# Kernel tuning notes

Hardware: AMD Instinct MI355X
Metric: run time of the kernel (lower is better)

The kernel has to match this reference:

```python
import jax, jax.numpy as jnp
import numpy as np

N, E = 10000, 640000
IN_FT, OUT_FT = 512, 128
NEG_SLOPE = 0.2


def setup_inputs() -> dict:
    key = jax.random.key(0)
    ks = jax.random.split(key, 10)
    seq = jax.random.normal(ks[0], (N, IN_FT), dtype=jnp.float32)
    # edges with no self-loops: dst = (src + offset) % N, offset in [1, N-1]
    src = jax.random.randint(ks[1], (E,), 0, N)
    off = jax.random.randint(ks[2], (E,), 1, N)
    dst = (src + off) % N
    edge_index = jnp.stack([src, dst]).astype(jnp.int64)
    # parameters (xavier-ish scale)
    W_fc = jax.random.normal(ks[3], (OUT_FT, IN_FT), dtype=jnp.float32) * (1.0 / np.sqrt(IN_FT))
    W_gat = jax.random.normal(ks[4], (OUT_FT, OUT_FT), dtype=jnp.float32) * (1.0 / np.sqrt(OUT_FT))
    att_src = jax.random.normal(ks[5], (OUT_FT,), dtype=jnp.float32) * 0.1
    att_dst = jax.random.normal(ks[6], (OUT_FT,), dtype=jnp.float32) * 0.1
    gat_bias = jnp.zeros((OUT_FT,), dtype=jnp.float32)
    bias = jnp.zeros((OUT_FT,), dtype=jnp.float32)
    prelu_a = jnp.asarray(0.25, dtype=jnp.float32)
    return {"seq": seq, "edge_index": edge_index, "W_fc": W_fc, "W_gat": W_gat,
            "att_src": att_src, "att_dst": att_dst, "gat_bias": gat_bias,
            "bias": bias, "prelu_a": prelu_a}


def _gat_forward(seq, src, dst, W_fc, W_gat, att_src, att_dst, gat_bias, bias, prelu_a):
    n = seq.shape[0]
    x = seq @ W_fc.T                      # [N, out_ft] fc (no bias)
    h = x @ W_gat.T                       # GATConv internal linear (no bias)
    a_s = h @ att_src                     # [N] per-node src attention logits
    a_d = h @ att_dst                     # [N]
    e = a_s[src] + a_d[dst]               # [E'] per-edge raw score
    e = jnp.where(e >= 0, e, NEG_SLOPE * e)
    # segment softmax over destination node
    m = jax.ops.segment_max(e, dst, num_segments=n)
    m = jnp.where(jnp.isfinite(m), m, 0.0)
    p = jnp.exp(e - m[dst])
    denom = jax.ops.segment_sum(p, dst, num_segments=n)
    alpha = p / (denom[dst] + 1e-16)
    msgs = alpha[:, None] * h[src]        # [E', out_ft]
    out = jax.ops.segment_sum(msgs, dst, num_segments=n) + gat_bias
    out = out + bias
    return jnp.where(out >= 0, out, prelu_a * out)  # PReLU


def reference(seq, edge_index, W_fc, W_gat, att_src, att_dst, gat_bias, bias, prelu_a):
    n = seq.shape[0]
    loops = jnp.arange(n, dtype=edge_index.dtype)   # add_self_loops
    src = jnp.concatenate([edge_index[0], loops])
    dst = jnp.concatenate([edge_index[1], loops])
    return _gat_forward(seq, src, dst, W_fc, W_gat, att_src, att_dst, gat_bias, bias, prelu_a)
```

## Files before the change

kernel.cpp:

```cpp
#include <hip/hip_runtime.h>
#include <hip/hip_bf16.h>

#define IN_FT 512
#define OUT_FT 128
#define NEG_SLOPE 0.2f
#define SHIFT_C 4.0f
#define CAP8 768
#define SEGC 128
#define NBMAX 1280

typedef __attribute__((ext_vector_type(8))) short short8;
typedef __attribute__((ext_vector_type(4))) short short4v;
typedef __attribute__((ext_vector_type(4))) float float4v;

__device__ inline short f2bf_s(float x) {
    __hip_bfloat16 b = __float2bfloat16(x);
    union { __hip_bfloat16 b; short s; } u;
    u.b = b;
    return u.s;
}
__device__ inline float bf2f(short s) {
    union { float f; unsigned u; } u;
    u.u = ((unsigned)(unsigned short)s) << 16;
    return u.f;
}

__global__ void k_prep(const float* __restrict__ Wg,
                       const float* __restrict__ Wf,
                       short* __restrict__ whf,
                       int* __restrict__ gcur, int nb) {
    if (blockIdx.x >= 256) {
        int i = (blockIdx.x - 256) * 256 + threadIdx.x;
        if (i < nb) gcur[i] = 0;
        return;
    }
    int idx = blockIdx.x * blockDim.x + threadIdx.x;
    int o = idx >> 9;
    int k = idx & 511;
    float s = 0.f;
#pragma unroll 8
    for (int j = 0; j < OUT_FT; ++j)
        s += Wg[o * OUT_FT + j] * Wf[j * IN_FT + k];
    int t = o >> 4, l15 = o & 15;
    int kc = k >> 5, q = (k >> 3) & 3, jj = k & 7;
    whf[(((kc * 8 + t) * 64) + q * 16 + l15) * 8 + jj] = f2bf_s(s);
}

__launch_bounds__(256)
__global__ void k_main(const float* __restrict__ seq,
                       const short8* __restrict__ whf,
                       const float* __restrict__ att_s_v,
                       const float* __restrict__ att_d_v,
                       short* __restrict__ h16,
                       float* __restrict__ a_s,
                       float* __restrict__ a_d,
                       const int* __restrict__ src,
                       const int* __restrict__ dstv,
                       int* __restrict__ gcur,
                       unsigned* __restrict__ bins,
                       int N, int E, int nb, int GB) {
    __shared__ char smem[24576];
    if (blockIdx.x >= GB) {
        int* hist  = (int*)smem;
        int* sbase = hist + NBMAX;
        int* scur  = sbase + NBMAX;
        int e0 = (blockIdx.x - GB) * 2048;
        for (int t = threadIdx.x; t < nb; t += 256) hist[t] = 0;
        __syncthreads();
        int myd[8];
#pragma unroll
        for (int k = 0; k < 8; ++k) {
            int e = e0 + k * 256 + threadIdx.x;
            myd[k] = (e < E) ? dstv[e] : -1;
            if ((unsigned)myd[k] < (unsigned)N) atomicAdd(&hist[myd[k] >> 3], 1);
            else myd[k] = -1;
        }
        __syncthreads();
        for (int t = threadIdx.x; t < nb; t += 256) {
            int c = hist[t];
            sbase[t] = c ? atomicAdd(&gcur[t], c) : 0;
            scur[t] = 0;
        }
        __syncthreads();
#pragma unroll
        for (int k = 0; k < 8; ++k) {
            if (myd[k] >= 0) {
                int e = e0 + k * 256 + threadIdx.x;
                int b = myd[k] >> 3;
                int slot = sbase[b] + atomicAdd(&scur[b], 1);
                if (slot < CAP8) {
                    int s = src[e];
                    if ((unsigned)s >= (unsigned)N) s = 0;
                    bins[(size_t)b * CAP8 + slot] = ((unsigned)s << 3) | (myd[k] & 7);
                }
            }
        }
        return;
    }
    short* As = (short*)smem;
    float4v* red = (float4v*)smem;

    int wave = threadIdx.x >> 6;
    int lane = threadIdx.x & 63;
    int l15 = lane & 15, quad = lane >> 4;
    int rows0 = blockIdx.x * 16;

#pragma unroll
    for (int i = 0; i < 8; ++i) {
        int idx = threadIdx.x + 256 * i;
        int r = idx >> 7, c4 = idx & 127;
        int row = rows0 + r;
        int rowc = row < N ? row : N - 1;
        float4 v = *(const float4*)(seq + (size_t)rowc * IN_FT + c4 * 4);
        short4v b;
        b[0] = f2bf_s(v.x); b[1] = f2bf_s(v.y); b[2] = f2bf_s(v.z); b[3] = f2bf_s(v.w);
        int kc = c4 >> 3, q = (c4 >> 1) & 3, half = c4 & 1;
        *(short4v*)(As + (((kc * 4 + q) * 16 + r) * 8 + half * 4)) = b;
    }
    __syncthreads();

    float4v acc[8];
    for (int t = 0; t < 8; ++t) acc[t] = (float4v){0.f, 0.f, 0.f, 0.f};

#pragma unroll
    for (int kk = 0; kk < 4; ++kk) {
        int kc = wave * 4 + kk;
        short8 a = *(const short8*)(As + ((kc * 4 + quad) * 16 + l15) * 8);
        const short8* bhp = whf + (size_t)kc * 512 + lane;
#pragma unroll
        for (int t = 0; t < 8; ++t) {
            short8 bh = bhp[t * 64];
            acc[t] = __builtin_amdgcn_mfma_f32_16x16x32_bf16(a, bh, acc[t], 0, 0, 0);
        }
    }
    __syncthreads();
    if (wave > 0) {
        float4v* base = red + ((wave - 1) * 8) * 64 + lane;
        for (int t = 0; t < 8; ++t) base[t * 64] = acc[t];
    }
    __syncthreads();
    if (wave != 0) return;
    for (int w2 = 0; w2 < 3; ++w2) {
        const float4v* base = red + (w2 * 8) * 64 + lane;
        for (int t = 0; t < 8; ++t) {
            float4v v = base[t * 64];
            acc[t][0] += v[0]; acc[t][1] += v[1]; acc[t][2] += v[2]; acc[t][3] += v[3];
        }
    }
    int rbase = rows0 + quad * 4;
    for (int r = 0; r < 4; ++r) {
        int rr = rbase + r;
        if (rr < N) {
            short* hr = h16 + (size_t)rr * OUT_FT;
            for (int t = 0; t < 8; ++t) hr[t * 16 + l15] = f2bf_s(acc[t][r]);
        }
    }
    float asv[8], adv[8];
    for (int t = 0; t < 8; ++t) {
        asv[t] = att_s_v[t * 16 + l15];
        adv[t] = att_d_v[t * 16 + l15];
    }
    for (int r = 0; r < 4; ++r) {
        float ps = 0.f, pd = 0.f;
        for (int t = 0; t < 8; ++t) {
            float v = acc[t][r];
            ps += v * asv[t];
            pd += v * adv[t];
        }
        for (int m = 1; m < 16; m <<= 1) {
            ps += __shfl_xor(ps, m);
            pd += __shfl_xor(pd, m);
        }
        int rr = rbase + r;
        if (l15 == 0 && rr < N) { a_s[rr] = ps; a_d[rr] = pd; }
    }
}

__launch_bounds__(256, 5)
__global__ void k_agg(const short* __restrict__ h16, const float* __restrict__ a_s,
                      const float* __restrict__ a_d,
                      const int* __restrict__ gcur, const unsigned* __restrict__ bins,
                      const float* __restrict__ gat_bias,
                      const float* __restrict__ bias,
                      const float* __restrict__ prelu_a,
                      float* __restrict__ out, int N) {
    __shared__ int2  seg[8][SEGC];
    __shared__ int   cur8[8], padn[8];
    __shared__ float ads[8];
    int b = blockIdx.x;
    int d0 = b << 3;
    int nd = N - d0; if (nd > 8) nd = 8;
    int tid = threadIdx.x;

    if (tid < 8) {
        cur8[tid] = 0;
        ads[tid] = (tid < nd) ? a_d[d0 + tid] : 0.f;
    }
    __syncthreads();

    int cnt = gcur[b]; if (cnt > CAP8) cnt = CAP8;
    const unsigned* binp = bins + (size_t)b * CAP8;

    for (int c = tid; c < cnt; c += 256) {
        unsigned pk = binp[c];
        int dl = pk & 7, sv = pk >> 3;
        float ev = a_s[sv] + ads[dl];
        ev = (ev >= 0.f) ? ev : NEG_SLOPE * ev;
        float p = __expf(ev - SHIFT_C);
        int slot = atomicAdd(&cur8[dl], 1);
        if (slot < SEGC) {
            int2 sp; sp.x = sv; sp.y = __float_as_int(p);
            seg[dl][slot] = sp;
        }
    }
    __syncthreads();
    if (tid < 8) {
        int n = cur8[tid]; if (n > SEGC) n = SEGC;
        int np = (n + 15) & ~15; if (np > SEGC) np = SEGC;
        padn[tid] = np;
    }
    __syncthreads();
    {
        int dl = tid >> 5, k = tid & 31;
        if (dl < 8) {
            int n = cur8[dl]; if (n > SEGC) n = SEGC;
            int np = padn[dl];
            if (n + k < np) {
                int2 sp; sp.x = d0; sp.y = 0;
                seg[dl][n + k] = sp;
            }
        }
    }
    __syncthreads();

    int w = tid >> 6, L = tid & 63;
    float b0 = gat_bias[2 * L] + bias[2 * L];
    float b1 = gat_bias[2 * L + 1] + bias[2 * L + 1];
    float pa = prelu_a[0];

    int dA = d0 + w, dB = d0 + w + 4;
    int dAc = dA < N ? dA : d0, dBc = dB < N ? dB : d0;
    float eA = a_s[dAc] + ads[w];
    eA = (eA >= 0.f) ? eA : NEG_SLOPE * eA;
    float p0A = __expf(eA - SHIFT_C);
    float eB = a_s[dBc] + ads[(w + 4) & 7];
    eB = (eB >= 0.f) ? eB : NEG_SLOPE * eB;
    float p0B = __expf(eB - SHIFT_C);
    short2 hA = *(const short2*)(h16 + (size_t)dAc * OUT_FT + 2 * L);
    short2 hB = *(const short2*)(h16 + (size_t)dBc * OUT_FT + 2 * L);
    float accA0 = p0A * bf2f(hA.x), accA1 = p0A * bf2f(hA.y), dsA = 0.f;
    float accB0 = p0B * bf2f(hB.x), accB1 = p0B * bf2f(hB.y), dsB = 0.f;

    const int2* segA = seg[w];
    const int2* segB = seg[w + 4];
    int nA = padn[w], nB = padn[w + 4];
    int nmax = nA > nB ? nA : nB;

    for (int c = 0; c < nmax; c += 16) {
        float ppA[16], ppB[16]; short2 hhA[16], hhB[16];
        bool doA = c < nA, doB = c < nB;
        if (doA) {
#pragma unroll
            for (int j = 0; j < 16; ++j) {
                int2 sp = segA[c + j];
                ppA[j] = __int_as_float(sp.y);
                hhA[j] = *(const short2*)(h16 + (size_t)sp.x * OUT_FT + 2 * L);
            }
        }
        if (doB) {
#pragma unroll
            for (int j = 0; j < 16; ++j) {
                int2 sp = segB[c + j];
                ppB[j] = __int_as_float(sp.y);
                hhB[j] = *(const short2*)(h16 + (size_t)sp.x * OUT_FT + 2 * L);
            }
        }
        if (doA) {
#pragma unroll
            for (int j = 0; j < 16; ++j) {
                dsA += ppA[j];
                accA0 += ppA[j] * bf2f(hhA[j].x);
                accA1 += ppA[j] * bf2f(hhA[j].y);
            }
        }
        if (doB) {
#pragma unroll
            for (int j = 0; j < 16; ++j) {
                dsB += ppB[j];
                accB0 += ppB[j] * bf2f(hhB[j].x);
                accB1 += ppB[j] * bf2f(hhB[j].y);
            }
        }
    }
    if (dA < N) {
        float inv = 1.f / (dsA + p0A + 1e-16f);
        float o0 = accA0 * inv + b0;
        float o1 = accA1 * inv + b1;
        o0 = (o0 >= 0.f) ? o0 : pa * o0;
        o1 = (o1 >= 0.f) ? o1 : pa * o1;
        float2 ov; ov.x = o0; ov.y = o1;
        *(float2*)(out + (size_t)dA * OUT_FT + 2 * L) = ov;
    }
    if (dB < N) {
        float inv = 1.f / (dsB + p0B + 1e-16f);
        float o0 = accB0 * inv + b0;
        float o1 = accB1 * inv + b1;
        o0 = (o0 >= 0.f) ? o0 : pa * o0;
        o1 = (o1 >= 0.f) ? o1 : pa * o1;
        float2 ov; ov.x = o0; ov.y = o1;
        *(float2*)(out + (size_t)dB * OUT_FT + 2 * L) = ov;
    }
}

extern "C" void kernel_launch(void* const* d_in, const int* in_sizes, int n_in,
                              void* d_out, int out_size, void* d_ws, size_t ws_size,
                              hipStream_t stream) {
    const float* seq     = (const float*)d_in[0];
    const int*   ei      = (const int*)d_in[1];
    const float* W_fc    = (const float*)d_in[2];
    const float* W_gat   = (const float*)d_in[3];
    const float* att_src = (const float*)d_in[4];
    const float* att_dst = (const float*)d_in[5];
    const float* gat_b   = (const float*)d_in[6];
    const float* bias    = (const float*)d_in[7];
    const float* prelu_a = (const float*)d_in[8];

    int N = in_sizes[0] / IN_FT;
    int E = in_sizes[1] / 2;
    const int* src = ei;
    const int* dst = ei + E;
    int nb = (N + 7) >> 3;

    char* wsb = (char*)d_ws;
    size_t cur = 0;
    auto alloc = [&](size_t bytes) -> void* {
        void* p = (void*)(wsb + cur);
        cur += (bytes + 255) & ~(size_t)255;
        return p;
    };
    short*    h16  = (short*)alloc((size_t)N * OUT_FT * 2);
    float*    a_s  = (float*)alloc((size_t)N * 4);
    float*    a_d  = (float*)alloc((size_t)N * 4);
    int*      gcur = (int*)alloc((size_t)nb * 4);
    unsigned* bins = (unsigned*)alloc((size_t)nb * CAP8 * 4);
    short*    whf  = (short*)alloc((size_t)OUT_FT * IN_FT * 2);

    int GB = (N + 15) / 16;
    int PB = (E + 2047) / 2048;

    k_prep<<<dim3(256 + (nb + 255) / 256), dim3(256), 0, stream>>>(W_gat, W_fc, whf, gcur, nb);
    k_main<<<dim3(GB + PB), dim3(256), 0, stream>>>(
        seq, (const short8*)whf, att_src, att_dst, h16, a_s, a_d,
        src, dst, gcur, bins, N, E, nb, GB);
    k_agg<<<dim3(nb), dim3(256), 0, stream>>>(
        h16, a_s, a_d, gcur, bins, gat_b, bias, prelu_a, (float*)d_out, N);
}
```

Baseline: 140.6 us.

## Software-pipeline gather loop in k_agg with double-buffered 8-edge chunks

Restructures the aggregation loop so that loads for the next 8-edge chunk are issued before accumulating the current chunk, using two register buffers per destination. The goal is to overlap gather latency with FMA work. It also merges the padding setup into a single phase, removing one barrier, and drops the min-blocks occupancy hint from the launch bounds. Dropping the hint may let register use rise and occupancy fall.

```diff
diff --git a/kernel.cpp b/kernel.cpp
--- a/kernel.cpp
+++ b/kernel.cpp
@@ -176,7 +176,7 @@
     }
 }
 
-__launch_bounds__(256, 5)
+__launch_bounds__(256)
 __global__ void k_agg(const short* __restrict__ h16, const float* __restrict__ a_s,
                       const float* __restrict__ a_d,
                       const int* __restrict__ gcur, const unsigned* __restrict__ bins,
@@ -214,21 +214,14 @@
         }
     }
     __syncthreads();
-    if (tid < 8) {
-        int n = cur8[tid]; if (n > SEGC) n = SEGC;
+    if (tid < 128) {
+        int dl = tid >> 4, k = tid & 15;
+        int n = cur8[dl]; if (n > SEGC) n = SEGC;
         int np = (n + 15) & ~15; if (np > SEGC) np = SEGC;
-        padn[tid] = np;
-    }
-    __syncthreads();
-    {
-        int dl = tid >> 5, k = tid & 31;
-        if (dl < 8) {
-            int n = cur8[dl]; if (n > SEGC) n = SEGC;
-            int np = padn[dl];
-            if (n + k < np) {
-                int2 sp; sp.x = d0; sp.y = 0;
-                seg[dl][n + k] = sp;
-            }
+        if (k == 0) padn[dl] = np;
+        if (n + k < np) {
+            int2 sp; sp.x = d0; sp.y = 0;
+            seg[dl][n + k] = sp;
         }
     }
     __syncthreads();
@@ -256,42 +249,45 @@
     int nA = padn[w], nB = padn[w + 4];
     int nmax = nA > nB ? nA : nB;
 
+    float pA0[8], pA1[8], pB0[8], pB1[8];
+    short2 hA0[8], hA1[8], hB0[8], hB1[8];
+
+#define LOADSEG(SEG, CC, PP, HH)                                          \
+    {                                                                     \
+        _Pragma("unroll")                                                 \
+        for (int j = 0; j < 8; ++j) {                                     \
+            int2 sp = (SEG)[(CC) + j];                                    \
+            PP[j] = __int_as_float(sp.y);                                 \
+            HH[j] = *(const short2*)(h16 + (size_t)sp.x * OUT_FT + 2 * L);\
+        }                                                                 \
+    }
+#define ACCUM(PP, HH, DS, A0, A1)                                         \
+    {                                                                     \
+        _Pragma("unroll")                                                 \
+        for (int j = 0; j < 8; ++j) {                                     \
+            DS += PP[j];                                                  \
+            A0 += PP[j] * bf2f(HH[j].x);                                  \
+            A1 += PP[j] * bf2f(HH[j].y);                                  \
+        }                                                                 \
+    }
+
+    if (0 < nA) LOADSEG(segA, 0, pA0, hA0)
+    if (0 < nB) LOADSEG(segB, 0, pB0, hB0)
     for (int c = 0; c < nmax; c += 16) {
-        float ppA[16], ppB[16]; short2 hhA[16], hhB[16];
-        bool doA = c < nA, doB = c < nB;
-        if (doA) {
-#pragma unroll
-            for (int j = 0; j < 16; ++j) {
-                int2 sp = segA[c + j];
-                ppA[j] = __int_as_float(sp.y);
-                hhA[j] = *(const short2*)(h16 + (size_t)sp.x * OUT_FT + 2 * L);
-            }
-        }
-        if (doB) {
-#pragma unroll
-            for (int j = 0; j < 16; ++j) {
-                int2 sp = segB[c + j];
-                ppB[j] = __int_as_float(sp.y);
-                hhB[j] = *(const short2*)(h16 + (size_t)sp.x * OUT_FT + 2 * L);
-            }
-        }
-        if (doA) {
-#pragma unroll
-            for (int j = 0; j < 16; ++j) {
-                dsA += ppA[j];
-                accA0 += ppA[j] * bf2f(hhA[j].x);
-                accA1 += ppA[j] * bf2f(hhA[j].y);
-            }
-        }
-        if (doB) {
-#pragma unroll
-            for (int j = 0; j < 16; ++j) {
-                dsB += ppB[j];
-                accB0 += ppB[j] * bf2f(hhB[j].x);
-                accB1 += ppB[j] * bf2f(hhB[j].y);
-            }
-        }
-    }
+        bool a1 = (c + 8) < nA, b1 = (c + 8) < nB;
+        bool a2 = (c + 16) < nA, b2 = (c + 16) < nB;
+        if (a1) LOADSEG(segA, c + 8, pA1, hA1)
+        if (b1) LOADSEG(segB, c + 8, pB1, hB1)
+        if (c < nA) ACCUM(pA0, hA0, dsA, accA0, accA1)
+        if (c < nB) ACCUM(pB0, hB0, dsB, accB0, accB1)
+        if (a2) LOADSEG(segA, c + 16, pA0, hA0)
+        if (b2) LOADSEG(segB, c + 16, pB0, hB0)
+        if (a1) ACCUM(pA1, hA1, dsA, accA0, accA1)
+        if (b1) ACCUM(pB1, hB1, dsB, accB0, accB1)
+    }
+#undef LOADSEG
+#undef ACCUM
+
     if (dA < N) {
         float inv = 1.f / (dsA + p0A + 1e-16f);
         float o0 = accA0 * inv + b0;
```

Result: faster. 135.5 us (-3.7%).
